# Optimization experiments

Hardware: AMD Instinct MI355X
Metric: run time of the kernel (lower is better)

## Reference

```python
import jax, jax.numpy as jnp
import numpy as np
from jax import lax

OUT_BINS = 256  # final time slice [:, :, :, :256, :]

def setup_inputs() -> dict:
    key = jax.random.key(0)
    k1, k2 = jax.random.split(key)
    B, X, Y, T = 8, 128, 128, 256
    data = jax.random.uniform(k1, (B, X, Y, T, 1), dtype=jnp.float32)
    irf = jax.random.uniform(k2, (B, 1, 1, T, 1), dtype=jnp.float32)
    return {"data": data, "irf": irf}

def _full_conv1d(sig_b, ker_b):
    # sig_b: [X, Y, T], ker_b: [T]. Full (polynomial) convolution along time,
    # which is exactly stride-1 VALID conv3d_transpose with a [1,1,T,1,1] kernel.
    X, Y, T = sig_b.shape
    lhs = sig_b.reshape(X * Y, 1, T)              # [N, C=1, W]
    rhs = ker_b[::-1].reshape(1, 1, T)            # flip -> true convolution
    out = lax.conv_general_dilated(lhs, rhs, window_strides=(1,), padding=[(T - 1, T - 1)])
    return out.reshape(X, Y, 2 * T - 1)

def reference(data, irf):
    B, X, Y, T, _ = data.shape
    k = irf.reshape(B, T)
    # per-sample kernel normalization: k / max(k)
    k = k / jnp.max(k, axis=1, keepdims=True)
    out = jax.vmap(_full_conv1d)(data[..., 0], k)  # [B, X, Y, 2T-1]
    return out[..., :OUT_BINS][..., None]          # [B, X, Y, 256, 1]
```

## Files before the change

### kernel.cpp

```cpp
#include <hip/hip_runtime.h>


typedef __attribute__((ext_vector_type(8))) short short8;
typedef __attribute__((ext_vector_type(4))) float floatx4;

#define T_BINS 256
#define PIX_PER_B (128 * 128)

__device__ inline unsigned short f2bf(float f) {
    unsigned int u = __float_as_uint(f);
    u += 0x7fffu + ((u >> 16) & 1u);
    return (unsigned short)(u >> 16);
}

__global__ __launch_bounds__(256) void build_W(const float* __restrict__ irf,
                                               unsigned short* __restrict__ W) {
    __shared__ float red[256];
    __shared__ float knorm[256];
    const int b = blockIdx.x;
    const int t = threadIdx.x;
    float v = irf[b * T_BINS + t];
    red[t] = v;
    __syncthreads();
    for (int s = 128; s > 0; s >>= 1) {
        if (t < s) red[t] = fmaxf(red[t], red[t + s]);
        __syncthreads();
    }
    knorm[t] = v / red[0];
    __syncthreads();
    unsigned short* Wb = W + b * 8192;
#pragma unroll
    for (int i = 0; i < 32; i++) {
        int e = i * 256 + t;
        int d  = e >> 9;
        int np = (e >> 5) & 15;
        int kl = e & 31;
        int idx = 16 * d + np - kl;
        Wb[e] = (idx >= 0) ? f2bf(knorm[idx]) : (unsigned short)0;
    }
}

__device__ inline short8 cvt_a(float4 lo, float4 hi) {
    short8 a;
    a[0] = (short)f2bf(lo.x); a[1] = (short)f2bf(lo.y);
    a[2] = (short)f2bf(lo.z); a[3] = (short)f2bf(lo.w);
    a[4] = (short)f2bf(hi.x); a[5] = (short)f2bf(hi.y);
    a[6] = (short)f2bf(hi.z); a[7] = (short)f2bf(hi.w);
    return a;
}

__global__ __launch_bounds__(256, 4) void conv_gemm(const float* __restrict__ data,
                                                    const unsigned short* __restrict__ W,
                                                    float* __restrict__ out) {
    const int b = blockIdx.x >> 8;
    const int mt = blockIdx.x & 255;
    const int t = threadIdx.x;
    const int w = t >> 6;
    const int l = t & 63;
    const int lq = l >> 4;
    const int lm = l & 15;

    __shared__ unsigned short Bs[8192];
    {
        const short8* src = (const short8*)(W + b * 8192);
        short8* dst = (short8*)Bs;
#pragma unroll
        for (int i = 0; i < 4; i++)
            dst[i * 256 + t] = src[i * 256 + t];
    }

    const int row = mt * 64 + w * 16 + lm;
    const float* Arow = data + ((size_t)b * PIX_PER_B + row) * T_BINS;

    float4 fbuf[4][2];
#pragma unroll
    for (int kk = 0; kk < 4; kk++) {
        fbuf[kk][0] = *(const float4*)(Arow + kk * 32 + lq * 8);
        fbuf[kk][1] = *(const float4*)(Arow + kk * 32 + lq * 8 + 4);
    }

    __syncthreads();

    float* Orow = out + ((size_t)b * PIX_PER_B + row) * T_BINS;
    const unsigned short* BsLane = Bs + lm * 32 + lq * 8;

    short8 af[8];

#pragma unroll
    for (int kk = 0; kk < 8; kk++) {
        const int cb = kk & 3;
        af[kk] = cvt_a(fbuf[cb][0], fbuf[cb][1]);
        if (kk + 4 < 8) {
            fbuf[cb][0] = *(const float4*)(Arow + (kk + 4) * 32 + lq * 8);
            fbuf[cb][1] = *(const float4*)(Arow + (kk + 4) * 32 + lq * 8 + 4);
        }
#pragma unroll
        for (int jo = 0; jo < 2; jo++) {
            const int j = 2 * kk + jo;
            floatx4 acc = (floatx4){0.f, 0.f, 0.f, 0.f};
#pragma unroll
            for (int k2 = 0; k2 <= kk; k2++) {
                const int d = j - 2 * k2;
                short8 bf = *(const short8*)(BsLane + d * 512);
                acc = __builtin_amdgcn_mfma_f32_16x16x32_bf16(bf, af[k2],
                                                              acc, 0, 0, 0);
            }
            *reinterpret_cast<floatx4*>(Orow + 16 * j + 4 * lq) = acc;
        }
    }
}

extern "C" void kernel_launch(void* const* d_in, const int* in_sizes, int n_in,
                              void* d_out, int out_size, void* d_ws, size_t ws_size,
                              hipStream_t stream) {
    const float* data = (const float*)d_in[0];
    const float* irf  = (const float*)d_in[1];
    float* outp = (float*)d_out;
    unsigned short* W = (unsigned short*)d_ws;

    build_W<<<8, 256, 0, stream>>>(irf, W);
    conv_gemm<<<2048, 256, 0, stream>>>(data, W, outp);
}
```

Baseline: 243.8 us.

## Stream A tiles and W into LDS via global_load_lds with double buffering

Replaces the per-thread register prefetch of the data rows and the register-staged copy of W with direct global-to-LDS DMA loads (global_load_lds). The A chunks go into a double-buffered LDS area with an XOR swizzle, so the next k-chunk loads while the current one is converted and fed to MFMA. It also raises occupancy hints to 5 waves per SIMD by freeing registers. In exchange it adds a per-iteration workgroup barrier, hand-placed vmcnt waits and 32KB of LDS per block.

```diff
diff --git a/kernel.cpp b/kernel.cpp
--- a/kernel.cpp
+++ b/kernel.cpp
@@ -6,6 +6,13 @@
 
 #define T_BINS 256
 #define PIX_PER_B (128 * 128)
+
+typedef __attribute__((address_space(3))) void lds_void;
+typedef __attribute__((address_space(1))) const void gbl_void;
+
+__device__ __forceinline__ void gload_lds16(const void* g, void* l) {
+    __builtin_amdgcn_global_load_lds((gbl_void*)g, (lds_void*)l, 16, 0, 0);
+}
 
 __device__ inline unsigned short f2bf(float f) {
     unsigned int u = __float_as_uint(f);
@@ -49,9 +56,12 @@
     return a;
 }
 
-__global__ __launch_bounds__(256, 4) void conv_gemm(const float* __restrict__ data,
+__global__ __launch_bounds__(256, 5) void conv_gemm(const float* __restrict__ data,
                                                     const unsigned short* __restrict__ W,
                                                     float* __restrict__ out) {
+    __shared__ alignas(16) unsigned char ldsb[32768];
+    unsigned short* Bs = (unsigned short*)ldsb;
+
     const int b = blockIdx.x >> 8;
     const int mt = blockIdx.x & 255;
     const int t = threadIdx.x;
@@ -60,52 +70,65 @@
     const int lq = l >> 4;
     const int lm = l & 15;
 
-    __shared__ unsigned short Bs[8192];
-    {
-        const short8* src = (const short8*)(W + b * 8192);
-        short8* dst = (short8*)Bs;
+    const float* Ab = data + ((size_t)b * PIX_PER_B + mt * 64) * T_BINS;
+    const int u0 = t,       r0 = u0 >> 3, c0 = (u0 & 7) ^ (r0 & 7);
+    const int u1 = 256 + t, r1 = u1 >> 3, c1 = (u1 & 7) ^ (r1 & 7);
+    const float* asrc0 = Ab + r0 * T_BINS + c0 * 4;
+    const float* asrc1 = Ab + r1 * T_BINS + c1 * 4;
+    const int admaoff = w * 1024;
+
+    gload_lds16(asrc0, ldsb + 16384 + admaoff);
+    gload_lds16(asrc1, ldsb + 16384 + 4096 + admaoff);
+    const unsigned short* Wb = W + b * 8192;
 #pragma unroll
-        for (int i = 0; i < 4; i++)
-            dst[i * 256 + t] = src[i * 256 + t];
-    }
-
-    const int row = mt * 64 + w * 16 + lm;
-    const float* Arow = data + ((size_t)b * PIX_PER_B + row) * T_BINS;
-
-    float4 fbuf[4][2];
-#pragma unroll
-    for (int kk = 0; kk < 4; kk++) {
-        fbuf[kk][0] = *(const float4*)(Arow + kk * 32 + lq * 8);
-        fbuf[kk][1] = *(const float4*)(Arow + kk * 32 + lq * 8 + 4);
-    }
-
+    for (int i = 0; i < 4; i++)
+        gload_lds16(Wb + (i * 256 + t) * 8, ldsb + i * 4096 + admaoff);
     __syncthreads();
 
-    float* Orow = out + ((size_t)b * PIX_PER_B + row) * T_BINS;
+    const int e = lm & 7;
+    const int rr = w * 16 + lm;
+    const int a_off0 = (rr * 8 + ((2 * lq) ^ e)) * 16;
+    const int a_off1 = (rr * 8 + ((2 * lq + 1) ^ e)) * 16;
     const unsigned short* BsLane = Bs + lm * 32 + lq * 8;
+    float* Orow = out + ((size_t)b * PIX_PER_B + mt * 64 + rr) * T_BINS;
 
     short8 af[8];
 
 #pragma unroll
     for (int kk = 0; kk < 8; kk++) {
-        const int cb = kk & 3;
-        af[kk] = cvt_a(fbuf[cb][0], fbuf[cb][1]);
-        if (kk + 4 < 8) {
-            fbuf[cb][0] = *(const float4*)(Arow + (kk + 4) * 32 + lq * 8);
-            fbuf[cb][1] = *(const float4*)(Arow + (kk + 4) * 32 + lq * 8 + 4);
+        if (kk < 7) {
+            const float* s0 = asrc0 + (kk + 1) * 32;
+            const float* s1 = asrc1 + (kk + 1) * 32;
+            unsigned char* dd = ldsb + 16384 + (((kk + 1) & 1) ? 8192 : 0) + admaoff;
+            gload_lds16(s0, dd);
+            gload_lds16(s1, dd + 4096);
         }
+        __builtin_amdgcn_sched_barrier(0);
+
+        const unsigned char* abase = ldsb + 16384 + ((kk & 1) ? 8192 : 0);
+        float4 lo = *(const float4*)(abase + a_off0);
+        float4 hi = *(const float4*)(abase + a_off1);
+        af[kk] = cvt_a(lo, hi);
+
 #pragma unroll
         for (int jo = 0; jo < 2; jo++) {
             const int j = 2 * kk + jo;
             floatx4 acc = (floatx4){0.f, 0.f, 0.f, 0.f};
 #pragma unroll
             for (int k2 = 0; k2 <= kk; k2++) {
-                const int d = j - 2 * k2;
-                short8 bf = *(const short8*)(BsLane + d * 512);
+                const int d2 = j - 2 * k2;
+                short8 bf = *(const short8*)(BsLane + d2 * 512);
                 acc = __builtin_amdgcn_mfma_f32_16x16x32_bf16(bf, af[k2],
                                                               acc, 0, 0, 0);
             }
             *reinterpret_cast<floatx4*>(Orow + 16 * j + 4 * lq) = acc;
+        }
+        __builtin_amdgcn_sched_barrier(0);
+
+        if (kk < 7) {
+            asm volatile("s_waitcnt vmcnt(2)" ::: "memory");
+            __builtin_amdgcn_s_barrier();
+            __builtin_amdgcn_sched_barrier(0);
         }
     }
 }
```

New measurement: 245.3 us. Within noise of the previous version (+0.6%).
